# Optimization experiments

Hardware: AMD Instinct MI355X
Metric: run time of the kernel (lower is better)

The kernel has to match this reference:

```python
import jax, jax.numpy as jnp
import numpy as np

NUM_HEADS = 8
AGENT_NUM = 64
THETA = 0.7


def conv2d(x, w, pad, groups=1):
    return jax.lax.conv_general_dilated(
        x, w, window_strides=(1, 1), padding=[(pad, pad), (pad, pad)],
        dimension_numbers=("NCHW", "OIHW", "NCHW"), feature_group_count=groups)


def setup_inputs() -> dict:
    key = jax.random.key(0)
    ks = jax.random.split(key, 8)
    B, C, H, W = 8, 256, 64, 64
    return {
        "x": jax.random.normal(ks[0], (B, C, H, W), jnp.float32),
        "qkv_w": jax.random.normal(ks[1], (3 * C, C, 3, 3), jnp.float32) * 0.05,
        "qkv_s": 1.0 + 0.05 * jax.random.normal(ks[2], (3 * C,), jnp.float32),
        "qkv_b": 0.05 * jax.random.normal(ks[3], (3 * C,), jnp.float32),
        "pe_w": jax.random.normal(ks[4], (C, 1, 3, 3), jnp.float32) * 0.05,
        "pe_s": 1.0 + 0.05 * jax.random.normal(ks[5], (C,), jnp.float32),
        "pe_b": 0.05 * jax.random.normal(ks[5], (C,), jnp.float32),
        "proj_w": jax.random.normal(ks[6], (C, C, 1, 1), jnp.float32) * 0.05,
        "proj_s": 1.0 + 0.05 * jax.random.normal(ks[7], (C,), jnp.float32),
        "proj_b": 0.05 * jax.random.normal(ks[7], (C,), jnp.float32),
    }


def reference(x, qkv_w, qkv_s, qkv_b, pe_w, pe_s, pe_b, proj_w, proj_s, proj_b):
    B, C, H, W = x.shape
    h, n = NUM_HEADS, AGENT_NUM
    d = C // h
    scale = d ** -0.5
    ps = int(n ** 0.5)  # pool_size = 8

    # Conv_dif (mode='hv'): normal 3x3 conv minus theta * (1x1 conv with hv-summed weights)
    out_n = conv2d(x, qkv_w, pad=1)
    dif_w = qkv_w.reshape(3 * C, C, 9)[:, :, jnp.array([1, 3, 4, 5, 7])].sum(-1)[:, :, None, None]
    out_d = conv2d(x, dif_w, pad=0)
    qkv = (out_n - THETA * out_d) * qkv_s[:, None, None] + qkv_b[:, None, None]  # folded BN

    q, k, v = jnp.split(qkv, 3, axis=1)  # each [B, C, H, W]
    qh = q.reshape(B, h, d, H * W)
    kh = k.reshape(B, h, d, H * W)
    vh = v.reshape(B, h, d, H * W)

    # adaptive avg pool q -> agent tokens (exact block mean since H,W % ps == 0)
    a = q.reshape(B, C, ps, H // ps, ps, W // ps).mean(axis=(3, 5))  # [B, C, ps, ps]
    a = a.reshape(B, C, n).transpose(0, 2, 1).reshape(B, n, h, d).transpose(0, 2, 3, 1)  # [B,h,d,n]

    # stage 1: agents attend to keys, aggregate values
    attn_k = jax.nn.softmax(jnp.einsum("bhdn,bhdN->bhnN", a, kh) * scale, axis=-1)
    attn = jnp.einsum("bhnN,bhdN->bhnd", attn_k, vh)  # [B,h,n,d]

    # stage 2: queries attend to agents
    q_attn = jax.nn.softmax(jnp.einsum("bhdN,bhdn->bhNn", qh, a) * scale, axis=-1)
    out = jnp.einsum("bhNn,bhnd->bhdN", q_attn, attn).reshape(B, C, H, W)

    # depthwise positional encoding on v (BN folded)
    pe = conv2d(v, pe_w, pad=1, groups=C) * pe_s[:, None, None] + pe_b[:, None, None]
    out = out + pe

    # 1x1 projection (BN folded, Identity act)
    out = conv2d(out, proj_w, pad=0) * proj_s[:, None, None] + proj_b[:, None, None]
    return out
```

## Files before the change

### kernel.cpp

```cpp
#include <hip/hip_runtime.h>
#include <cstdint>

typedef __attribute__((ext_vector_type(8))) short short8;
typedef __attribute__((ext_vector_type(4))) float f32x4;

#define THETA 0.7f
#define SCALE 0.17677669529663687f

__device__ __forceinline__ ushort f2b(float f) {
    uint32_t u = __float_as_uint(f);
    u += 0x7FFFu + ((u >> 16) & 1u);
    return (ushort)(u >> 16);
}
__device__ __forceinline__ float b2f(ushort b) {
    return __uint_as_float(((uint32_t)b) << 16);
}

__global__ __launch_bounds__(256) void k_pad(const float* __restrict__ x, ushort* __restrict__ xp) {
    int b = blockIdx.x >> 6, y = blockIdx.x & 63;
    int t = threadIdx.x;
    __shared__ float buf[64][65];
    for (int cc = 0; cc < 4; ++cc) {
        __syncthreads();
#pragma unroll
        for (int i = 0; i < 16; ++i) {
            int idx = i * 256 + t;
            int c = idx >> 6, xx = idx & 63;
            buf[c][xx] = x[(((size_t)b * 256 + cc * 64 + c) << 12) + (y << 6) + xx];
        }
        __syncthreads();
#pragma unroll
        for (int i = 0; i < 16; ++i) {
            int idx = i * 256 + t;
            int xx = idx >> 6, c = idx & 63;
            xp[((size_t)(b * 66 + y + 1) * 66 + (xx + 1)) * 256 + cc * 64 + c] = f2b(buf[c][xx]);
        }
    }
}

__global__ __launch_bounds__(256) void k_foldw(const float* __restrict__ w, const float* __restrict__ s,
                                               ushort* __restrict__ Wa) {
    int o = blockIdx.x, c = threadIdx.x;
    const float* wp = w + ((size_t)o * 256 + c) * 9;
    float v[9];
#pragma unroll
    for (int p = 0; p < 9; ++p) v[p] = wp[p];
    float hv = v[1] + v[3] + v[4] + v[5] + v[7];
    v[4] -= THETA * hv;
    float sc = s[o];
#pragma unroll
    for (int p = 0; p < 9; ++p)
        Wa[(size_t)o * 2304 + p * 256 + c] = f2b(v[p] * sc);
}

__global__ __launch_bounds__(256) void k_foldp(const float* __restrict__ w, const float* __restrict__ s,
                                               ushort* __restrict__ Wh, ushort* __restrict__ Wl) {
    int o = blockIdx.x, c = threadIdx.x;
    float v = w[(size_t)o * 256 + c] * s[o];
    ushort hi = f2b(v);
    Wh[(size_t)o * 256 + c] = hi;
    Wl[(size_t)o * 256 + c] = f2b(v - b2f(hi));
}

__global__ __launch_bounds__(256) void k_conv(const ushort* __restrict__ xp, const ushort* __restrict__ Wa,
                                              const float* __restrict__ qbias, ushort* __restrict__ qkv) {
    __shared__ ushort Al[128][40];
    __shared__ ushort Bl[128][40];
    const int t = threadIdx.x;
    const int bid0 = blockIdx.x;
    const int bid = (bid0 & 7) * 192 + (bid0 >> 3);
    const int b = bid / 192;
    const int ob = (bid % 192) >> 5;
    const int pb = bid & 31;
    const int o0 = ob << 7;
    const int lane = t & 63;
    const int w = t >> 6;
    const int rw = t >> 2;
    const int q4 = t & 3;
    const ushort* Ag0 = Wa + (size_t)(o0 + rw) * 2304 + q4 * 8;
    const ushort* Ag1 = Ag0 + (size_t)64 * 2304;
    const int y0 = pb * 2;
    const size_t xb = (size_t)b * 66 * 66 * 256;

    f32x4 acc[4][4] = {};

    const int ow2 = (w >> 1) << 6;
    const int pw2 = (w & 1) << 6;
    const int fr = lane & 15;
    const int fs = (lane >> 4) << 3;

    uint4 ra0, ra1, rb0, rb1;
    auto loadk = [&](int kn) {
        int pp = kn >> 3;
        int c0 = (kn & 7) << 5;
        int ky = pp / 3, kx = pp - ky * 3;
        ra0 = *(const uint4*)(Ag0 + kn * 32);
        ra1 = *(const uint4*)(Ag1 + kn * 32);
        const ushort* bp = xp + xb + ((size_t)((y0 + ky) * 66 + (rw + kx))) * 256 + c0 + q4 * 8;
        rb0 = *(const uint4*)bp;
        rb1 = *(const uint4*)(bp + 66 * 256);
    };
    loadk(0);
    for (int kc = 0; kc < 72; ++kc) {
        if (kc) __syncthreads();
        *(uint4*)&Al[rw][q4 * 8] = ra0;
        *(uint4*)&Al[rw + 64][q4 * 8] = ra1;
        *(uint4*)&Bl[rw][q4 * 8] = rb0;
        *(uint4*)&Bl[rw + 64][q4 * 8] = rb1;
        __syncthreads();
        if (kc < 71) loadk(kc + 1);
        short8 af[4], bf[4];
#pragma unroll
        for (int i = 0; i < 4; ++i) af[i] = *(const short8*)&Al[ow2 + i * 16 + fr][fs];
#pragma unroll
        for (int j = 0; j < 4; ++j) bf[j] = *(const short8*)&Bl[pw2 + j * 16 + fr][fs];
#pragma unroll
        for (int i = 0; i < 4; ++i)
#pragma unroll
            for (int j = 0; j < 4; ++j)
                acc[i][j] = __builtin_amdgcn_mfma_f32_16x16x32_bf16(af[i], bf[j], acc[i][j], 0, 0, 0);
    }
    const int pbase = pb * 128 + pw2 + (lane & 15);
#pragma unroll
    for (int i = 0; i < 4; ++i) {
        int o = o0 + ow2 + i * 16 + (lane >> 4) * 4;
#pragma unroll
        for (int r = 0; r < 4; ++r) {
            float bias = qbias[o + r];
            ushort* dst = qkv + ((size_t)b * 768 + o + r) * 4096 + pbase;
#pragma unroll
            for (int j = 0; j < 4; ++j)
                dst[j * 16] = f2b(acc[i][j][r] + bias);
        }
    }
}

__global__ __launch_bounds__(256) void k_pool(const ushort* __restrict__ qkv, float* __restrict__ ap) {
    const int bid = blockIdx.x;
    const int b = bid >> 8, c = bid & 255;
    const int t = threadIdx.x;
    const int y = t >> 2, xq = t & 3;
    __shared__ float lp[64][8];
    const ushort* qp = qkv + ((size_t)b * 768 + c) * 4096 + y * 64 + xq * 16;
    short8 a0 = *(const short8*)(qp);
    short8 a1 = *(const short8*)(qp + 8);
    float s0 = 0, s1 = 0;
#pragma unroll
    for (int j = 0; j < 8; ++j) s0 += b2f((ushort)a0[j]);
#pragma unroll
    for (int j = 0; j < 8; ++j) s1 += b2f((ushort)a1[j]);
    lp[y][xq * 2] = s0;
    lp[y][xq * 2 + 1] = s1;
    __syncthreads();
    if (t < 64) {
        int py = t >> 3, px = t & 7;
        float s = 0;
#pragma unroll
        for (int r = 0; r < 8; ++r) s += lp[py * 8 + r][px];
        ap[((size_t)b * 256 + c) * 64 + t] = s * (1.0f / 64.0f);
    }
}

__global__ __launch_bounds__(256) void k_att1(const ushort* __restrict__ qkv, const float* __restrict__ ap,
                                              float* __restrict__ attn_g, float* __restrict__ s_g) {
    const int bid0 = blockIdx.x;
    const int bid = (bid0 & 7) * 64 + (bid0 >> 3);
    const int seg = bid & 7, h = (bid >> 3) & 7, b = bid >> 6;
    const int t = threadIdx.x;
    __shared__ float a_s[64][36];
    __shared__ ushort EL[256][68];
    __shared__ ushort vL[256][40];
#pragma unroll
    for (int i = 0; i < 8; ++i) {
        int idx = i * 256 + t;
        int n = idx & 63, d = idx >> 6;
        a_s[n][d] = ap[((size_t)b * 256 + h * 32 + d) * 64 + n] * SCALE;
    }
    const ushort* kb = qkv + ((size_t)b * 768 + 256 + h * 32) * 4096;
    const ushort* vb = qkv + ((size_t)b * 768 + 512 + h * 32) * 4096;
    const int n_own = t >> 2;
    const int dl = t & 3;
    float accr[8] = {0, 0, 0, 0, 0, 0, 0, 0};
    float s_acc = 0.f;
    __syncthreads();
    for (int chunk = 0; chunk < 2; ++chunk) {
        int pix = (seg * 2 + chunk) * 256 + t;
        float kr[32];
#pragma unroll
        for (int d = 0; d < 32; ++d) kr[d] = b2f(kb[(size_t)d * 4096 + pix]);
#pragma unroll
        for (int i = 0; i < 4; ++i) {
            uint4 pk;
            pk.x = (uint32_t)vb[(size_t)(8 * i + 0) * 4096 + pix] |
                   ((uint32_t)vb[(size_t)(8 * i + 1) * 4096 + pix] << 16);
            pk.y = (uint32_t)vb[(size_t)(8 * i + 2) * 4096 + pix] |
                   ((uint32_t)vb[(size_t)(8 * i + 3) * 4096 + pix] << 16);
            pk.z = (uint32_t)vb[(size_t)(8 * i + 4) * 4096 + pix] |
                   ((uint32_t)vb[(size_t)(8 * i + 5) * 4096 + pix] << 16);
            pk.w = (uint32_t)vb[(size_t)(8 * i + 6) * 4096 + pix] |
                   ((uint32_t)vb[(size_t)(8 * i + 7) * 4096 + pix] << 16);
            *(uint4*)&vL[t][i * 8] = pk;
        }
#pragma unroll 1
        for (int np = 0; np < 32; ++np) {
            float l0 = 0, l1 = 0;
#pragma unroll
            for (int dq = 0; dq < 8; ++dq) {
                f32x4 a0 = *(const f32x4*)&a_s[2 * np][dq * 4];
                f32x4 a1 = *(const f32x4*)&a_s[2 * np + 1][dq * 4];
                l0 += a0.x * kr[dq * 4] + a0.y * kr[dq * 4 + 1] + a0.z * kr[dq * 4 + 2] + a0.w * kr[dq * 4 + 3];
                l1 += a1.x * kr[dq * 4] + a1.y * kr[dq * 4 + 1] + a1.z * kr[dq * 4 + 2] + a1.w * kr[dq * 4 + 3];
            }
            uint32_t e2 = (uint32_t)f2b(__expf(l0)) | ((uint32_t)f2b(__expf(l1)) << 16);
            *(uint32_t*)&EL[t][2 * np] = e2;
        }
        __syncthreads();
#pragma unroll 1
        for (int tt = 0; tt < 256; ++tt) {
            float e = b2f(EL[tt][n_own]);
            if (dl == 0) s_acc += e;
            ushort4 va = *(const ushort4*)&vL[tt][dl * 8];
            ushort4 vbx = *(const ushort4*)&vL[tt][dl * 8 + 4];
            accr[0] += e * b2f(va.x);
            accr[1] += e * b2f(va.y);
            accr[2] += e * b2f(va.z);
            accr[3] += e * b2f(va.w);
            accr[4] += e * b2f(vbx.x);
            accr[5] += e * b2f(vbx.y);
            accr[6] += e * b2f(vbx.z);
            accr[7] += e * b2f(vbx.w);
        }
        __syncthreads();
    }
#pragma unroll
    for (int i = 0; i < 8; ++i)
        atomicAdd(&attn_g[(((size_t)b * 8 + h) * 64 + n_own) * 32 + dl * 8 + i], accr[i]);
    if (dl == 0) atomicAdd(&s_g[((size_t)b * 8 + h) * 64 + n_own], s_acc);
}

__global__ __launch_bounds__(256, 2) void k_att2(const ushort* __restrict__ qkv, const float* __restrict__ ap,
                                                 const float* __restrict__ attn_g, const float* __restrict__ s_g,
                                                 ushort* __restrict__ outp) {
    const int bid0 = blockIdx.x;
    const int bid = (bid0 & 7) * 256 + (bid0 >> 3);
    const int ch = bid & 31, h = (bid >> 5) & 7, b = bid >> 8;
    const int t = threadIdx.x;
    const int lane = t & 63, w = t >> 6;
    const int fr = lane & 15, fs = (lane >> 4) << 3;
    const int pw = w << 5;
    const int pix0 = ch << 7;

    __shared__ ushort a_lds[64][40];
    __shared__ ushort qt[128][40];
    __shared__ ushort pt[128][72];
    __shared__ ushort gh[32][72];
    __shared__ ushort gl[32][72];
    __shared__ float sInv[64];

#pragma unroll
    for (int i = 0; i < 8; ++i) {
        int e = i * 256 + t;
        int n = e & 63, d = e >> 6;
        a_lds[n][d] = f2b(ap[((size_t)b * 256 + h * 32 + d) * 64 + n] * SCALE);
    }
    if (t < 64) sInv[t] = 1.0f / s_g[((size_t)b * 8 + h) * 64 + t];
#pragma unroll
    for (int i = 0; i < 2; ++i) {
        int e = i * 256 + t;
        int d = e & 31, oc = e >> 5;
        const ushort* src = qkv + ((size_t)b * 768 + h * 32 + d) * 4096 + pix0 + oc * 8;
        short8 v = *(const short8*)src;
#pragma unroll
        for (int j2 = 0; j2 < 8; ++j2) qt[oc * 8 + j2][d] = (ushort)v[j2];
    }
    __syncthreads();

#pragma unroll
    for (int i = 0; i < 8; ++i) {
        int e = i * 256 + t;
        int n = e >> 5, d = e & 31;
        float g = attn_g[(((size_t)b * 8 + h) * 64 + n) * 32 + d] * sInv[n];
        ushort hi = f2b(g);
        gh[d][n] = hi;
        gl[d][n] = f2b(g - b2f(hi));
    }

    f32x4 accL[4][2];
    {
        short8 af[4], bq[2];
#pragma unroll
        for (int i = 0; i < 4; ++i) af[i] = *(const short8*)&a_lds[i * 16 + fr][fs];
#pragma unroll
        for (int j = 0; j < 2; ++j) bq[j] = *(const short8*)&qt[pw + j * 16 + fr][fs];
#pragma unroll
        for (int i = 0; i < 4; ++i)
#pragma unroll
            for (int j = 0; j < 2; ++j) {
                f32x4 z = {0.f, 0.f, 0.f, 0.f};
                accL[i][j] = __builtin_amdgcn_mfma_f32_16x16x32_bf16(af[i], bq[j], z, 0, 0, 0);
            }
    }
    float sj[2];
#pragma unroll
    for (int j = 0; j < 2; ++j) {
        float s = 0.f;
        int pix = pw + j * 16 + fr;
#pragma unroll
        for (int i = 0; i < 4; ++i) {
            float e0 = __expf(accL[i][j][0]);
            float e1 = __expf(accL[i][j][1]);
            float e2 = __expf(accL[i][j][2]);
            float e3 = __expf(accL[i][j][3]);
            s += (e0 + e1) + (e2 + e3);
            int n0 = i * 16 + (lane >> 4) * 4;
            *(uint32_t*)&pt[pix][n0] = (uint32_t)f2b(e0) | ((uint32_t)f2b(e1) << 16);
            *(uint32_t*)&pt[pix][n0 + 2] = (uint32_t)f2b(e2) | ((uint32_t)f2b(e3) << 16);
        }
        s += __shfl_xor(s, 16);
        s += __shfl_xor(s, 32);
        sj[j] = 1.0f / s;
    }
    __syncthreads();

    f32x4 accO[2][2] = {};
#pragma unroll
    for (int ks = 0; ks < 2; ++ks) {
        short8 gah[2], gal[2], pa[2];
#pragma unroll
        for (int dt = 0; dt < 2; ++dt) {
            gah[dt] = *(const short8*)&gh[dt * 16 + fr][ks * 32 + fs];
            gal[dt] = *(const short8*)&gl[dt * 16 + fr][ks * 32 + fs];
        }
#pragma unroll
        for (int j = 0; j < 2; ++j) pa[j] = *(const short8*)&pt[pw + j * 16 + fr][ks * 32 + fs];
#pragma unroll
        for (int dt = 0; dt < 2; ++dt)
#pragma unroll
            for (int j = 0; j < 2; ++j) {
                accO[dt][j] = __builtin_amdgcn_mfma_f32_16x16x32_bf16(gah[dt], pa[j], accO[dt][j], 0, 0, 0);
                accO[dt][j] = __builtin_amdgcn_mfma_f32_16x16x32_bf16(gal[dt], pa[j], accO[dt][j], 0, 0, 0);
            }
    }
#pragma unroll
    for (int dt = 0; dt < 2; ++dt)
#pragma unroll
        for (int j = 0; j < 2; ++j) {
            int pix = pix0 + pw + j * 16 + fr;
#pragma unroll
            for (int r = 0; r < 4; ++r) {
                int d = dt * 16 + (lane >> 4) * 4 + r;
                outp[((size_t)b * 256 + h * 32 + d) * 4096 + pix] = f2b(accO[dt][j][r] * sj[j]);
            }
        }
}

__global__ __launch_bounds__(256) void k_pe(const ushort* __restrict__ qkv, const float* __restrict__ pw,
                                            const float* __restrict__ ps, const float* __restrict__ pbias,
                                            ushort* __restrict__ outp) {
    int gid = blockIdx.x * 256 + threadIdx.x;
    int x4 = (gid & 15) << 2;
    int y = (gid >> 4) & 63;
    int c = (gid >> 10) & 255;
    int b = gid >> 18;
    const ushort* vp = qkv + ((size_t)b * 768 + 512 + c) * 4096;
    const float* wp = pw + c * 9;
    float s0 = 0, s1 = 0, s2 = 0, s3 = 0;
#pragma unroll
    for (int ky = 0; ky < 3; ++ky) {
        int yy = y + ky - 1;
        if ((unsigned)yy >= 64u) continue;
        const ushort* rp = vp + yy * 64 + x4;
        ushort4 m = *(const ushort4*)rp;
        float m0 = b2f(m.x), m1 = b2f(m.y), m2 = b2f(m.z), m3 = b2f(m.w);
        float lft = (x4 > 0) ? b2f(rp[-1]) : 0.f;
        float rgt = (x4 < 60) ? b2f(rp[4]) : 0.f;
        float w0 = wp[ky * 3], w1 = wp[ky * 3 + 1], w2 = wp[ky * 3 + 2];
        s0 += w0 * lft + w1 * m0 + w2 * m1;
        s1 += w0 * m0 + w1 * m1 + w2 * m2;
        s2 += w0 * m1 + w1 * m2 + w2 * m3;
        s3 += w0 * m2 + w1 * m3 + w2 * rgt;
    }
    float sc = ps[c], bb = pbias[c];
    ushort* op = outp + ((size_t)b * 256 + c) * 4096 + y * 64 + x4;
    ushort4 o = *(ushort4*)op;
    o.x = f2b(b2f(o.x) + sc * s0 + bb);
    o.y = f2b(b2f(o.y) + sc * s1 + bb);
    o.z = f2b(b2f(o.z) + sc * s2 + bb);
    o.w = f2b(b2f(o.w) + sc * s3 + bb);
    *(ushort4*)op = o;
}

__global__ __launch_bounds__(256) void k_proj(const ushort* __restrict__ outp, const ushort* __restrict__ Wh,
                                              const ushort* __restrict__ Wl, const float* __restrict__ pbias,
                                              float* __restrict__ out) {
    __shared__ ushort Ah[128][40];
    __shared__ ushort Alo[128][40];
    __shared__ ushort Xl[32][132];
    const int t = threadIdx.x;
    const int bid0 = blockIdx.x;
    const int bid = (bid0 & 7) * 64 + (bid0 >> 3);
    const int b = bid >> 6;
    const int ob = (bid >> 5) & 1;
    const int pb = bid & 31;
    const int o0 = ob << 7;
    const int p0 = pb << 7;
    const int lane = t & 63;
    const int w = t >> 6;
    const int rw = t >> 2, q4 = t & 3;
    const int cl = t >> 3, pg = t & 7;
    const int ow2 = (w >> 1) << 6;
    const int pw2 = (w & 1) << 6;
    const int fr = lane & 15;
    const int fs = (lane >> 4) << 3;

    f32x4 acc[4][4] = {};
    uint4 rah0, rah1, ral0, ral1, rx0, rx1;
    auto loadk = [&](int kc) {
        const size_t awoff = (size_t)(o0 + rw) * 256 + kc * 32 + q4 * 8;
        rah0 = *(const uint4*)(Wh + awoff);
        rah1 = *(const uint4*)(Wh + awoff + (size_t)64 * 256);
        ral0 = *(const uint4*)(Wl + awoff);
        ral1 = *(const uint4*)(Wl + awoff + (size_t)64 * 256);
        const ushort* xsrc = outp + ((size_t)b * 256 + kc * 32 + cl) * 4096 + p0 + pg * 16;
        rx0 = *(const uint4*)xsrc;
        rx1 = *(const uint4*)(xsrc + 8);
    };
    loadk(0);
    for (int kc = 0; kc < 8; ++kc) {
        if (kc) __syncthreads();
        *(uint4*)&Ah[rw][q4 * 8] = rah0;
        *(uint4*)&Ah[rw + 64][q4 * 8] = rah1;
        *(uint4*)&Alo[rw][q4 * 8] = ral0;
        *(uint4*)&Alo[rw + 64][q4 * 8] = ral1;
        *(uint4*)&Xl[cl][pg * 16] = rx0;
        *(uint4*)&Xl[cl][pg * 16 + 8] = rx1;
        __syncthreads();
        if (kc < 7) loadk(kc + 1);
        short8 ah[4], al[4], bf[4];
#pragma unroll
        for (int i = 0; i < 4; ++i) {
            ah[i] = *(const short8*)&Ah[ow2 + i * 16 + fr][fs];
            al[i] = *(const short8*)&Alo[ow2 + i * 16 + fr][fs];
        }
#pragma unroll
        for (int j = 0; j < 4; ++j) {
            int pl = pw2 + j * 16 + fr;
#pragma unroll
            for (int kk = 0; kk < 8; ++kk) bf[j][kk] = (short)Xl[fs + kk][pl];
        }
#pragma unroll
        for (int i = 0; i < 4; ++i)
#pragma unroll
            for (int j = 0; j < 4; ++j) {
                acc[i][j] = __builtin_amdgcn_mfma_f32_16x16x32_bf16(ah[i], bf[j], acc[i][j], 0, 0, 0);
                acc[i][j] = __builtin_amdgcn_mfma_f32_16x16x32_bf16(al[i], bf[j], acc[i][j], 0, 0, 0);
            }
    }
    const int pbase = p0 + pw2 + (lane & 15);
#pragma unroll
    for (int i = 0; i < 4; ++i) {
        int o = o0 + ow2 + i * 16 + (lane >> 4) * 4;
#pragma unroll
        for (int r = 0; r < 4; ++r) {
            float bias = pbias[o + r];
            float* dst = out + ((size_t)b * 256 + o + r) * 4096 + pbase;
#pragma unroll
            for (int j = 0; j < 4; ++j)
                dst[j * 16] = acc[i][j][r] + bias;
        }
    }
}

extern "C" void kernel_launch(void* const* d_in, const int* in_sizes, int n_in,
                              void* d_out, int out_size, void* d_ws, size_t ws_size,
                              hipStream_t stream) {
    const float* x = (const float*)d_in[0];
    const float* qkv_w = (const float*)d_in[1];
    const float* qkv_s = (const float*)d_in[2];
    const float* qkv_b = (const float*)d_in[3];
    const float* pe_w = (const float*)d_in[4];
    const float* pe_s = (const float*)d_in[5];
    const float* pe_b = (const float*)d_in[6];
    const float* proj_w = (const float*)d_in[7];
    const float* proj_s = (const float*)d_in[8];
    const float* proj_b = (const float*)d_in[9];
    float* out = (float*)d_out;

    char* ws = (char*)d_ws;
    ushort* xp = (ushort*)(ws);
    ushort* Wa = (ushort*)(ws + 17842176);
    ushort* qkvb = (ushort*)(ws + 21381120);
    float* apool = (float*)(ws + 71712768);
    float* attn_g = (float*)(ws + 72237056);
    float* s_g = (float*)(ws + 72761344);
    ushort* outpb = (ushort*)(ws + 72777728);
    ushort* Wh = (ushort*)(ws + 89554944);
    ushort* Wl = (ushort*)(ws + 89686016);

    hipMemsetAsync(xp, 0, 17842176, stream);
    hipMemsetAsync(attn_g, 0, 524288 + 16384, stream);
    k_pad<<<512, 256, 0, stream>>>(x, xp);
    k_foldw<<<768, 256, 0, stream>>>(qkv_w, qkv_s, Wa);
    k_foldp<<<256, 256, 0, stream>>>(proj_w, proj_s, Wh, Wl);
    k_conv<<<1536, 256, 0, stream>>>(xp, Wa, qkv_b, qkvb);
    k_pool<<<2048, 256, 0, stream>>>(qkvb, apool);
    k_att1<<<512, 256, 0, stream>>>(qkvb, apool, attn_g, s_g);
    k_att2<<<2048, 256, 0, stream>>>(qkvb, apool, attn_g, s_g, outpb);
    k_pe<<<8192, 256, 0, stream>>>(qkvb, pe_w, pe_s, pe_b, outpb);
    k_proj<<<512, 256, 0, stream>>>(outpb, Wh, Wl, proj_b, out);
}
```

Measured before the change: 408.0 us.

## Stage conv GEMM tiles via direct global-to-LDS loads with double buffering

Result: slower. 424.2 us (+4.0%).

```diff
diff --git a/kernel.cpp b/kernel.cpp
--- a/kernel.cpp
+++ b/kernel.cpp
@@ -14,6 +14,12 @@
 }
 __device__ __forceinline__ float b2f(ushort b) {
     return __uint_as_float(((uint32_t)b) << 16);
+}
+
+typedef const __attribute__((address_space(1))) uint32_t* gas1_t;
+typedef __attribute__((address_space(3))) uint32_t* las3_t;
+__device__ __forceinline__ void gload16(const ushort* g, ushort* l) {
+    __builtin_amdgcn_global_load_lds((gas1_t)g, (las3_t)l, 16, 0, 0);
 }
 
 __global__ __launch_bounds__(256) void k_pad(const float* __restrict__ x, ushort* __restrict__ xp) {
@@ -64,8 +70,8 @@
 
 __global__ __launch_bounds__(256) void k_conv(const ushort* __restrict__ xp, const ushort* __restrict__ Wa,
                                               const float* __restrict__ qbias, ushort* __restrict__ qkv) {
-    __shared__ ushort Al[128][40];
-    __shared__ ushort Bl[128][40];
+    __shared__ ushort Abuf[2][4096];
+    __shared__ ushort Bbuf[2][4096];
     const int t = threadIdx.x;
     const int bid0 = blockIdx.x;
     const int bid = (bid0 & 7) * 192 + (bid0 >> 3);
@@ -75,45 +81,48 @@
     const int o0 = ob << 7;
     const int lane = t & 63;
     const int w = t >> 6;
-    const int rw = t >> 2;
-    const int q4 = t & 3;
-    const ushort* Ag0 = Wa + (size_t)(o0 + rw) * 2304 + q4 * 8;
-    const ushort* Ag1 = Ag0 + (size_t)64 * 2304;
     const int y0 = pb * 2;
     const size_t xb = (size_t)b * 66 * 66 * 256;
 
+    const int lrow = lane >> 2;
+    const int lcol8 = (lane & 3) << 3;
+
+    const ushort* pA = Wa + (size_t)(o0 + w * 32 + lrow) * 2304 + lcol8;
+    const ushort* pB = xp + xb + (size_t)((w & 1) * 32 + lrow) * 256 + lcol8;
+    const int yrow = y0 + (w >> 1);
+
     f32x4 acc[4][4] = {};
-
     const int ow2 = (w >> 1) << 6;
     const int pw2 = (w & 1) << 6;
     const int fr = lane & 15;
     const int fs = (lane >> 4) << 3;
 
-    uint4 ra0, ra1, rb0, rb1;
-    auto loadk = [&](int kn) {
+    auto stage = [&](int kn, int buf) {
         int pp = kn >> 3;
         int c0 = (kn & 7) << 5;
-        int ky = pp / 3, kx = pp - ky * 3;
-        ra0 = *(const uint4*)(Ag0 + kn * 32);
-        ra1 = *(const uint4*)(Ag1 + kn * 32);
-        const ushort* bp = xp + xb + ((size_t)((y0 + ky) * 66 + (rw + kx))) * 256 + c0 + q4 * 8;
-        rb0 = *(const uint4*)bp;
-        rb1 = *(const uint4*)(bp + 66 * 256);
+        int ky = pp / 3;
+        int kx = pp - ky * 3;
+        const ushort* ga = pA + kn * 32;
+        const ushort* gb = pB + ((size_t)((yrow + ky) * 66 + kx)) * 256 + c0;
+        ushort* la = &Abuf[buf][w * 1024];
+        ushort* lb = &Bbuf[buf][w * 1024];
+        gload16(ga, la);
+        gload16(ga + 16 * 2304, la + 512);
+        gload16(gb, lb);
+        gload16(gb + 16 * 256, lb + 512);
     };
-    loadk(0);
-    for (int kc = 0; kc < 72; ++kc) {
-        if (kc) __syncthreads();
-        *(uint4*)&Al[rw][q4 * 8] = ra0;
-        *(uint4*)&Al[rw + 64][q4 * 8] = ra1;
-        *(uint4*)&Bl[rw][q4 * 8] = rb0;
-        *(uint4*)&Bl[rw + 64][q4 * 8] = rb1;
+
+    stage(0, 0);
+    for (int kn = 0; kn < 72; ++kn) {
         __syncthreads();
-        if (kc < 71) loadk(kc + 1);
+        if (kn < 71) stage(kn + 1, (kn + 1) & 1);
+        const ushort* Ac = Abuf[kn & 1];
+        const ushort* Bc = Bbuf[kn & 1];
         short8 af[4], bf[4];
 #pragma unroll
-        for (int i = 0; i < 4; ++i) af[i] = *(const short8*)&Al[ow2 + i * 16 + fr][fs];
-#pragma unroll
-        for (int j = 0; j < 4; ++j) bf[j] = *(const short8*)&Bl[pw2 + j * 16 + fr][fs];
+        for (int i = 0; i < 4; ++i) af[i] = *(const short8*)&Ac[(ow2 + i * 16 + fr) * 32 + fs];
+#pragma unroll
+        for (int j = 0; j < 4; ++j) bf[j] = *(const short8*)&Bc[(pw2 + j * 16 + fr) * 32 + fs];
 #pragma unroll
         for (int i = 0; i < 4; ++i)
 #pragma unroll
```

## Rewrite agent-key attention stage with bf16 MFMA for logits and value aggregation

Applied to the files above, without the earlier changes.

Result: faster. 390.1 us (-4.4%).

```diff
diff --git a/kernel.cpp b/kernel.cpp
--- a/kernel.cpp
+++ b/kernel.cpp
@@ -161,81 +161,118 @@
     }
 }
 
-__global__ __launch_bounds__(256) void k_att1(const ushort* __restrict__ qkv, const float* __restrict__ ap,
-                                              float* __restrict__ attn_g, float* __restrict__ s_g) {
+__global__ __launch_bounds__(256, 2) void k_att1(const ushort* __restrict__ qkv, const float* __restrict__ ap,
+                                                 float* __restrict__ attn_g, float* __restrict__ s_g) {
     const int bid0 = blockIdx.x;
-    const int bid = (bid0 & 7) * 64 + (bid0 >> 3);
-    const int seg = bid & 7, h = (bid >> 3) & 7, b = bid >> 6;
+    const int bid = (bid0 & 7) * 128 + (bid0 >> 3);
+    const int seg = bid & 15, h = (bid >> 4) & 7, b = bid >> 7;
     const int t = threadIdx.x;
-    __shared__ float a_s[64][36];
-    __shared__ ushort EL[256][68];
-    __shared__ ushort vL[256][40];
+    const int lane = t & 63, w = t >> 6;
+    const int fr = lane & 15, fs = (lane >> 4) << 3;
+    const int g4 = (lane >> 4) << 2;
+    const int pixseg = seg << 8;
+
+    __shared__ ushort a_lds[64][40];
+    __shared__ ushort kt[256][40];
+    __shared__ ushort pt[64][264];
+
 #pragma unroll
     for (int i = 0; i < 8; ++i) {
-        int idx = i * 256 + t;
-        int n = idx & 63, d = idx >> 6;
-        a_s[n][d] = ap[((size_t)b * 256 + h * 32 + d) * 64 + n] * SCALE;
+        int e = i * 256 + t;
+        int n = e & 63, d = e >> 6;
+        a_lds[n][d] = f2b(ap[((size_t)b * 256 + h * 32 + d) * 64 + n] * SCALE);
     }
     const ushort* kb = qkv + ((size_t)b * 768 + 256 + h * 32) * 4096;
     const ushort* vb = qkv + ((size_t)b * 768 + 512 + h * 32) * 4096;
-    const int n_own = t >> 2;
-    const int dl = t & 3;
-    float accr[8] = {0, 0, 0, 0, 0, 0, 0, 0};
-    float s_acc = 0.f;
+#pragma unroll
+    for (int i = 0; i < 4; ++i) {
+        int e = i * 256 + t;
+        int d = e & 31, oc = e >> 5;
+        const ushort* src = kb + (size_t)d * 4096 + pixseg + oc * 8;
+        short8 v = *(const short8*)src;
+#pragma unroll
+        for (int j2 = 0; j2 < 8; ++j2) kt[oc * 8 + j2][d] = (ushort)v[j2];
+    }
     __syncthreads();
-    for (int chunk = 0; chunk < 2; ++chunk) {
-        int pix = (seg * 2 + chunk) * 256 + t;
-        float kr[32];
-#pragma unroll
-        for (int d = 0; d < 32; ++d) kr[d] = b2f(kb[(size_t)d * 4096 + pix]);
-#pragma unroll
-        for (int i = 0; i < 4; ++i) {
-            uint4 pk;
-            pk.x = (uint32_t)vb[(size_t)(8 * i + 0) * 4096 + pix] |
-                   ((uint32_t)vb[(size_t)(8 * i + 1) * 4096 + pix] << 16);
-            pk.y = (uint32_t)vb[(size_t)(8 * i + 2) * 4096 + pix] |
-                   ((uint32_t)vb[(size_t)(8 * i + 3) * 4096 + pix] << 16);
-            pk.z = (uint32_t)vb[(size_t)(8 * i + 4) * 4096 + pix] |
-                   ((uint32_t)vb[(size_t)(8 * i + 5) * 4096 + pix] << 16);
-            pk.w = (uint32_t)vb[(size_t)(8 * i + 6) * 4096 + pix] |
-                   ((uint32_t)vb[(size_t)(8 * i + 7) * 4096 + pix] << 16);
-            *(uint4*)&vL[t][i * 8] = pk;
-        }
-#pragma unroll 1
-        for (int np = 0; np < 32; ++np) {
-            float l0 = 0, l1 = 0;
-#pragma unroll
-            for (int dq = 0; dq < 8; ++dq) {
-                f32x4 a0 = *(const f32x4*)&a_s[2 * np][dq * 4];
-                f32x4 a1 = *(const f32x4*)&a_s[2 * np + 1][dq * 4];
-                l0 += a0.x * kr[dq * 4] + a0.y * kr[dq * 4 + 1] + a0.z * kr[dq * 4 + 2] + a0.w * kr[dq * 4 + 3];
-                l1 += a1.x * kr[dq * 4] + a1.y * kr[dq * 4 + 1] + a1.z * kr[dq * 4 + 2] + a1.w * kr[dq * 4 + 3];
-            }
-            uint32_t e2 = (uint32_t)f2b(__expf(l0)) | ((uint32_t)f2b(__expf(l1)) << 16);
-            *(uint32_t*)&EL[t][2 * np] = e2;
-        }
-        __syncthreads();
-#pragma unroll 1
-        for (int tt = 0; tt < 256; ++tt) {
-            float e = b2f(EL[tt][n_own]);
-            if (dl == 0) s_acc += e;
-            ushort4 va = *(const ushort4*)&vL[tt][dl * 8];
-            ushort4 vbx = *(const ushort4*)&vL[tt][dl * 8 + 4];
-            accr[0] += e * b2f(va.x);
-            accr[1] += e * b2f(va.y);
-            accr[2] += e * b2f(va.z);
-            accr[3] += e * b2f(va.w);
-            accr[4] += e * b2f(vbx.x);
-            accr[5] += e * b2f(vbx.y);
-            accr[6] += e * b2f(vbx.z);
-            accr[7] += e * b2f(vbx.w);
-        }
-        __syncthreads();
-    }
-#pragma unroll
-    for (int i = 0; i < 8; ++i)
-        atomicAdd(&attn_g[(((size_t)b * 8 + h) * 64 + n_own) * 32 + dl * 8 + i], accr[i]);
-    if (dl == 0) atomicAdd(&s_g[((size_t)b * 8 + h) * 64 + n_own], s_acc);
+
+    f32x4 accL[4][4];
+    {
+        short8 af[4], bq[4];
+#pragma unroll
+        for (int i = 0; i < 4; ++i) af[i] = *(const short8*)&a_lds[i * 16 + fr][fs];
+#pragma unroll
+        for (int j = 0; j < 4; ++j) bq[j] = *(const short8*)&kt[w * 64 + j * 16 + fr][fs];
+#pragma unroll
+        for (int i = 0; i < 4; ++i)
+#pragma unroll
+            for (int j = 0; j < 4; ++j) {
+                f32x4 z = {0.f, 0.f, 0.f, 0.f};
+                accL[i][j] = __builtin_amdgcn_mfma_f32_16x16x32_bf16(af[i], bq[j], z, 0, 0, 0);
+            }
+    }
+    float sreg[4][4];
+#pragma unroll
+    for (int i = 0; i < 4; ++i)
+#pragma unroll
+        for (int r = 0; r < 4; ++r) sreg[i][r] = 0.f;
+#pragma unroll
+    for (int i = 0; i < 4; ++i)
+#pragma unroll
+        for (int j = 0; j < 4; ++j) {
+            int pixl = w * 64 + j * 16 + fr;
+#pragma unroll
+            for (int r = 0; r < 4; ++r) {
+                float e = __expf(accL[i][j][r]);
+                sreg[i][r] += e;
+                pt[i * 16 + g4 + r][pixl] = f2b(e);
+            }
+        }
+#pragma unroll
+    for (int i = 0; i < 4; ++i)
+#pragma unroll
+        for (int r = 0; r < 4; ++r) {
+            float s = sreg[i][r];
+            s += __shfl_xor(s, 1);
+            s += __shfl_xor(s, 2);
+            s += __shfl_xor(s, 4);
+            s += __shfl_xor(s, 8);
+            sreg[i][r] = s;
+        }
+    if (fr == 0) {
+#pragma unroll
+        for (int i = 0; i < 4; ++i)
+#pragma unroll
+            for (int r = 0; r < 4; ++r)
+                atomicAdd(&s_g[((size_t)b * 8 + h) * 64 + i * 16 + g4 + r], sreg[i][r]);
+    }
+    __syncthreads();
+
+    f32x4 accO[4][2] = {};
+#pragma unroll
+    for (int ks = 0; ks < 2; ++ks) {
+        int pixk = w * 64 + ks * 32 + fs;
+        short8 af[4], bf[2];
+#pragma unroll
+        for (int i = 0; i < 4; ++i) af[i] = *(const short8*)&pt[i * 16 + fr][pixk];
+#pragma unroll
+        for (int dt = 0; dt < 2; ++dt)
+            bf[dt] = *(const short8*)(vb + (size_t)(dt * 16 + fr) * 4096 + pixseg + pixk);
+#pragma unroll
+        for (int i = 0; i < 4; ++i)
+#pragma unroll
+            for (int dt = 0; dt < 2; ++dt)
+                accO[i][dt] = __builtin_amdgcn_mfma_f32_16x16x32_bf16(af[i], bf[dt], accO[i][dt], 0, 0, 0);
+    }
+#pragma unroll
+    for (int i = 0; i < 4; ++i)
+#pragma unroll
+        for (int dt = 0; dt < 2; ++dt)
+#pragma unroll
+            for (int r = 0; r < 4; ++r) {
+                int n = i * 16 + g4 + r;
+                int d = dt * 16 + fr;
+                atomicAdd(&attn_g[(((size_t)b * 8 + h) * 64 + n) * 32 + d], accO[i][dt][r]);
+            }
 }
 
 __global__ __launch_bounds__(256, 2) void k_att2(const ushort* __restrict__ qkv, const float* __restrict__ ap,
@@ -504,7 +541,7 @@
     k_foldp<<<256, 256, 0, stream>>>(proj_w, proj_s, Wh, Wl);
     k_conv<<<1536, 256, 0, stream>>>(xp, Wa, qkv_b, qkvb);
     k_pool<<<2048, 256, 0, stream>>>(qkvb, apool);
-    k_att1<<<512, 256, 0, stream>>>(qkvb, apool, attn_g, s_g);
+    k_att1<<<1024, 256, 0, stream>>>(qkvb, apool, attn_g, s_g);
     k_att2<<<2048, 256, 0, stream>>>(qkvb, apool, attn_g, s_g, outpb);
     k_pe<<<8192, 256, 0, stream>>>(qkvb, pe_w, pe_s, pe_b, outpb);
     k_proj<<<512, 256, 0, stream>>>(outpb, Wh, Wl, proj_b, out);
```
